# Kernel optimization log

Hardware: AMD Instinct MI355X
Metric: run time of the kernel (lower is better)

The kernel has to match this reference:

```python
import jax, jax.numpy as jnp
import numpy as np

N_HEADS = 16


def _rotate_half(x):
    x_even = x[..., ::2]
    x_odd = x[..., 1::2]
    return jnp.stack((-x_odd, x_even), axis=-1).reshape(x.shape)


def _apply_rope(x, cos, sin):
    # cos/sin: (S, d_head) broadcast against (B, H, S, d_head)
    return x * cos + _rotate_half(x) * sin


def setup_inputs() -> dict:
    key = jax.random.key(0)
    k1, k2, k3 = jax.random.split(key, 3)
    B, S, D, H = 2, 2048, 1024, N_HEADS
    dh = D // H
    x = jax.random.normal(k1, (B, S, D), dtype=jnp.float32)
    w_qkv = jax.random.normal(k2, (D, 3 * D), dtype=jnp.float32) * 0.02
    w_proj = jax.random.normal(k3, (D, D), dtype=jnp.float32) * 0.02
    # standard interleaved RoPE tables, shape (S, d_head)
    inv_freq = 1.0 / (10000.0 ** (jnp.arange(0, dh, 2, dtype=jnp.float32) / dh))
    angles = jnp.arange(S, dtype=jnp.float32)[:, None] * inv_freq[None, :]  # (S, dh/2)
    rope_cos = jnp.repeat(jnp.cos(angles), 2, axis=-1)  # (S, dh)
    rope_sin = jnp.repeat(jnp.sin(angles), 2, axis=-1)
    return {"x": x, "w_qkv": w_qkv, "w_proj": w_proj, "rope_cos": rope_cos, "rope_sin": rope_sin}


def reference(x, w_qkv, w_proj, rope_cos, rope_sin):
    B, S, D = x.shape
    H = N_HEADS
    dh = D // H
    half = dh // 2
    qkv = x @ w_qkv  # (B, S, 3D)
    q, k, v = jnp.split(qkv, 3, axis=-1)
    # (B, S, D) -> (B, H, S, dh)
    q = q.reshape(B, S, H, dh).transpose(0, 2, 1, 3)
    k = k.reshape(B, S, H, dh).transpose(0, 2, 1, 3)
    v = v.reshape(B, S, H, dh).transpose(0, 2, 1, 3)
    q = _apply_rope(q, rope_cos, rope_sin)
    k = _apply_rope(k, rope_cos, rope_sin)
    scale = half ** -0.5
    # dual score matrices from the two half-subspaces
    attn_up = jnp.einsum('bhid,bhjd->bhij', q[..., :half], k[..., :half]) * scale
    attn_down = jnp.einsum('bhid,bhjd->bhij', q[..., half:], k[..., half:]) * scale
    lower_mask = jnp.tril(jnp.ones((S, S), dtype=bool))  # j <= i -> down
    attn_logits = jnp.where(lower_mask, attn_down, attn_up)
    attn_weights = jax.nn.softmax(attn_logits, axis=-1)
    attn_out = jnp.einsum('bhij,bhjd->bhid', attn_weights, v)
    attn_out = attn_out.transpose(0, 2, 1, 3).reshape(B, S, D)
    return attn_out @ w_proj
```

## Files before the change

kernel.cpp:

```cpp
#include <hip/hip_runtime.h>
#include <hip/hip_bf16.h>
#include <stdint.h>

typedef __bf16 bf16;
typedef __attribute__((ext_vector_type(4))) __bf16 bf16x4;
typedef __attribute__((ext_vector_type(8))) __bf16 bf16x8;
typedef __attribute__((ext_vector_type(4))) float f32x4;

#define MFMA16(a, b, c) __builtin_amdgcn_mfma_f32_16x16x32_bf16((a), (b), (c), 0, 0, 0)

#define QSC (0.17677669529663687f * 1.4426950408889634f)

__device__ __forceinline__ void async_cp16(const bf16* g, bf16* l) {
  __builtin_amdgcn_global_load_lds(
      (const __attribute__((address_space(1))) void*)g,
      (__attribute__((address_space(3))) void*)l, 16, 0, 0);
}

__global__ __launch_bounds__(256) void convx_k(const float* __restrict__ in,
                                               bf16* __restrict__ out, int n) {
  int i = (blockIdx.x * 256 + threadIdx.x) * 4;
  const int stride = gridDim.x * 256 * 4;
  for (; i < n; i += stride) {
    const f32x4 f = *(const f32x4*)(in + i);
    bf16x4 o;
    o[0] = (bf16)f[0]; o[1] = (bf16)f[1]; o[2] = (bf16)f[2]; o[3] = (bf16)f[3];
    *(bf16x4*)(out + i) = o;
  }
}

__global__ __launch_bounds__(256) void transpose_k(const float* __restrict__ in,
                                                   bf16* __restrict__ out, int R, int C) {
  __shared__ bf16 t[64][65];
  const int bc = blockIdx.x * 64;
  const int br = blockIdx.y * 64;
  const int tx = threadIdx.x & 63, ty = threadIdx.x >> 6;
#pragma unroll
  for (int r = ty; r < 64; r += 4) t[r][tx] = (bf16)in[(br + r) * C + bc + tx];
  __syncthreads();
#pragma unroll
  for (int r = ty; r < 64; r += 4) out[(bc + r) * R + br + tx] = t[tx][r];
}

template <int MODE, int BM>
__global__ __launch_bounds__(256) void gemm128(
    const bf16* __restrict__ A, const bf16* __restrict__ BT, int M, int N, int K,
    float* __restrict__ C, bf16* __restrict__ qws, bf16* __restrict__ kws,
    bf16* __restrict__ vT, const float* __restrict__ ropeC, const float* __restrict__ ropeS) {
  constexpr int MT = BM / 32;
  __shared__ __align__(16) bf16 As[BM * 64];
  __shared__ __align__(16) bf16 Bs[128 * 64];
  const int tid = threadIdx.x;
  const int lane = tid & 63, wave = tid >> 6;
  const int l16 = lane & 15, quad = lane >> 4;
  const int wm = (wave >> 1) * (BM / 2), wn = (wave & 1) * 64;
  const int bm = blockIdx.y, bn = blockIdx.x;

  const int srow = tid >> 3;
  const int schunk = ((tid & 7) - srow) & 7;
  const bf16* ag = A + (bm * BM + srow) * K + schunk * 8;
  const bf16* bg = BT + (bn * 128 + srow) * K + schunk * 8;
  bf16* la = &As[tid * 8];
  bf16* lb = &Bs[tid * 8];

  f32x4 acc[MT][4] = {};

  for (int k0 = 0; k0 < K; k0 += 64) {
    async_cp16(ag + k0, la);
    async_cp16(ag + 32 * K + k0, la + 2048);
    if (BM == 128) {
      async_cp16(ag + 64 * K + k0, la + 4096);
      async_cp16(ag + 96 * K + k0, la + 6144);
    }
    async_cp16(bg + k0, lb);
    async_cp16(bg + 32 * K + k0, lb + 2048);
    async_cp16(bg + 64 * K + k0, lb + 4096);
    async_cp16(bg + 96 * K + k0, lb + 6144);
    __syncthreads();
#pragma unroll
    for (int ks = 0; ks < 2; ++ks) {
      bf16x8 af[MT], bff[4];
#pragma unroll
      for (int t = 0; t < MT; ++t) {
        const int r = wm + t * 16 + l16;
        af[t] = *(const bf16x8*)&As[r * 64 + ((ks * 4 + quad + r) & 7) * 8];
      }
#pragma unroll
      for (int t = 0; t < 4; ++t) {
        const int r = wn + t * 16 + l16;
        bff[t] = *(const bf16x8*)&Bs[r * 64 + ((ks * 4 + quad + r) & 7) * 8];
      }
#pragma unroll
      for (int mt = 0; mt < MT; ++mt)
#pragma unroll
        for (int nt = 0; nt < 4; ++nt) acc[mt][nt] = MFMA16(af[mt], bff[nt], acc[mt][nt]);
    }
    __syncthreads();
  }

  if (MODE == 0) {
#pragma unroll
    for (int mt = 0; mt < MT; ++mt)
#pragma unroll
      for (int i = 0; i < 4; ++i) {
        const int row = bm * BM + wm + mt * 16 + quad * 4 + i;
#pragma unroll
        for (int nt = 0; nt < 4; ++nt) {
          const int col = bn * 128 + wn + nt * 16 + l16;
          C[row * N + col] = acc[mt][nt][i];
        }
      }
  } else {
    bf16* tb = &Bs[wave * 512];
#pragma unroll
    for (int mt = 0; mt < MT; ++mt) {
      const int s0 = bm * BM + wm + mt * 16;
      const int b = s0 >> 11, sbase = s0 & 2047;
#pragma unroll
      for (int nt = 0; nt < 4; ++nt) {
        const int colb = bn * 128 + wn + nt * 16;
        const int sec = colb >> 10, rem = colb & 1023;
        const int h = rem >> 6, d0 = rem & 63;
        if (sec < 2) {
          const int d = d0 + l16;
#pragma unroll
          for (int i = 0; i < 4; ++i) {
            const int s = sbase + quad * 4 + i;
            float v = acc[mt][nt][i];
            float pr = __shfl_xor(v, 1);
            float rot = (d & 1) ? pr : -pr;
            float rv = v * ropeC[s * 64 + d] + rot * ropeS[s * 64 + d];
            if (sec == 0) rv *= QSC;
            tb[(quad * 4 + i) * 20 + l16] = (bf16)rv;
          }
          bf16* dst = ((sec == 0) ? qws : kws) + ((b * 16 + h) * 2048 + sbase) * 64 + d0;
          bf16x4 seg = *(const bf16x4*)&tb[l16 * 20 + quad * 4];
          *(bf16x4*)(dst + l16 * 64 + quad * 4) = seg;
        } else {
          const int d = d0 + l16;
          const int s4 = sbase + quad * 4;
          const int a = (s4 >> 4) & 3;
          const int p = (s4 & ~63) | ((a >> 1) * 32 + quad * 8 + (a & 1) * 4);
          bf16x4 pk;
#pragma unroll
          for (int i = 0; i < 4; ++i) pk[i] = (bf16)acc[mt][nt][i];
          *(bf16x4*)(vT + ((b * 16 + h) * 64 + d) * 2048 + p) = pk;
        }
      }
    }
  }
}

__global__ __launch_bounds__(256) void attn_k(const bf16* __restrict__ qws,
                                              const bf16* __restrict__ kws,
                                              const bf16* __restrict__ vT,
                                              bf16* __restrict__ aw) {
  __shared__ __align__(16) bf16 Ks[2][64 * 64];
  __shared__ __align__(16) bf16 Vs[2][64 * 64];
  const int tid = threadIdx.x;
  const int lane = tid & 63, wave = tid >> 6;
  const int l16 = lane & 15, quad = lane >> 4;
  const int bh = blockIdx.x >> 4, qblk = blockIdx.x & 15;
  const int b = bh >> 4, h = bh & 15;
  const int rbase = qblk * 128 + wave * 32;

  const bf16* qb = qws + (bh * 2048 + rbase) * 64;
  const bf16* kb = kws + bh * 2048 * 64;
  const bf16* vb = vT + bh * 64 * 2048;

  const int r0 = wave * 16 + (lane >> 3);
  const int c0 = ((lane & 7) - r0) & 7;
  const bf16* kst0 = kb + r0 * 64 + c0 * 8;
  const bf16* kst1 = kb + (r0 + 8) * 64 + c0 * 8;
  const bf16* vst0 = vb + r0 * 2048 + c0 * 8;
  const bf16* vst1 = vb + (r0 + 8) * 2048 + c0 * 8;

#define STAGE(jtv)                                         \
  {                                                        \
    bf16* kdst = &Ks[(jtv) & 1][wave * 1024];              \
    bf16* vdst = &Vs[(jtv) & 1][wave * 1024];              \
    async_cp16(kst0 + (jtv) * 4096, kdst);                 \
    async_cp16(kst1 + (jtv) * 4096, kdst + 512);           \
    async_cp16(vst0 + (jtv) * 64, vdst);                   \
    async_cp16(vst1 + (jtv) * 64, vdst + 512);             \
  }

  bf16x8 qf[2][2];
#pragma unroll
  for (int g = 0; g < 2; ++g)
#pragma unroll
    for (int hf = 0; hf < 2; ++hf)
      qf[g][hf] = *(const bf16x8*)(qb + (g * 16 + l16) * 64 + hf * 32 + quad * 8);

  bf16x8 ones;
#pragma unroll
  for (int j = 0; j < 8; ++j) ones[j] = (bf16)1.0f;

  f32x4 o[2][4] = {};
  f32x4 o_l[2] = {};
  const f32x4 zz = {};
  const int tdw = rbase >> 6;

#define ATTN_BODY(TM, jt)                                                             \
  {                                                                                   \
    const bf16* Kb = Ks[(jt) & 1];                                                    \
    const bf16* Vb = Vs[(jt) & 1];                                                    \
    bf16x8 vf[2][4];                                                                  \
    _Pragma("unroll") for (int ks = 0; ks < 2; ++ks)                                  \
      _Pragma("unroll") for (int ntd = 0; ntd < 4; ++ntd)                             \
        vf[ks][ntd] = *(const bf16x8*)(Vb + (ntd * 16 + l16) * 64 +                   \
                                       ((ks * 4 + quad + l16) & 7) * 8);              \
    bf16x8 kfU[2][2], kfD[2][2];                                                      \
    _Pragma("unroll") for (int ks = 0; ks < 2; ++ks)                                  \
      _Pragma("unroll") for (int s = 0; s < 2; ++s) {                                 \
        const int ro = ((ks * 2 + s) * 16 + l16) * 64;                                \
        if (TM != 0) kfU[ks][s] = *(const bf16x8*)(Kb + ro + ((quad + l16) & 7) * 8); \
        if (TM != 2)                                                                  \
          kfD[ks][s] = *(const bf16x8*)(Kb + ro + ((4 + quad + l16) & 7) * 8);        \
      }                                                                               \
    if ((jt) + 1 < 32) STAGE((jt) + 1)                                                \
    _Pragma("unroll") for (int ks = 0; ks < 2; ++ks) {                                \
      f32x4 sU[2][2], sD[2][2];                                                       \
      _Pragma("unroll") for (int s = 0; s < 2; ++s)                                   \
        _Pragma("unroll") for (int g = 0; g < 2; ++g) {                               \
          if (TM != 0) sU[s][g] = MFMA16(kfU[ks][s], qf[g][0], zz);                   \
          if (TM != 2) sD[s][g] = MFMA16(kfD[ks][s], qf[g][1], zz);                   \
        }                                                                             \
      _Pragma("unroll") for (int g = 0; g < 2; ++g) {                                 \
        bf16x8 af;                                                                    \
        _Pragma("unroll") for (int s = 0; s < 2; ++s)                                 \
          _Pragma("unroll") for (int r = 0; r < 4; ++r) {                             \
            float x;                                                                  \
            if (TM == 0) x = sD[s][g][r];                                             \
            else if (TM == 2) x = sU[s][g][r];                                        \
            else {                                                                    \
              const int jcol = (jt) * 64 + (ks * 2 + s) * 16 + quad * 4 + r;          \
              x = (jcol <= rbase + g * 16 + l16) ? sD[s][g][r] : sU[s][g][r];         \
            }                                                                         \
            af[s * 4 + r] = (bf16)__builtin_amdgcn_exp2f(x);                          \
          }                                                                           \
        o_l[g] = MFMA16(af, ones, o_l[g]);                                            \
        _Pragma("unroll") for (int ntd = 0; ntd < 4; ++ntd)                           \
            o[g][ntd] = MFMA16(af, vf[ks][ntd], o[g][ntd]);                           \
      }                                                                               \
    }                                                                                 \
  }

  STAGE(0)
  for (int jt = 0; jt < 32; ++jt) {
    asm volatile("s_waitcnt vmcnt(0)" ::: "memory");
    __syncthreads();
    if (jt < tdw) ATTN_BODY(0, jt)
    else if (jt == tdw) ATTN_BODY(1, jt)
    else ATTN_BODY(2, jt)
  }
#undef ATTN_BODY
#undef STAGE

#pragma unroll
  for (int g = 0; g < 2; ++g) {
    float ir[4];
#pragma unroll
    for (int r = 0; r < 4; ++r) ir[r] = __builtin_amdgcn_rcpf(o_l[g][r]);
#pragma unroll
    for (int ntd = 0; ntd < 4; ++ntd)
#pragma unroll
      for (int r = 0; r < 4; ++r)
        aw[(b * 2048 + rbase + g * 16 + quad * 4 + r) * 1024 + h * 64 + ntd * 16 + l16] =
            (bf16)(o[g][ntd][r] * ir[r]);
  }
}

extern "C" void kernel_launch(void* const* d_in, const int* in_sizes, int n_in,
                              void* d_out, int out_size, void* d_ws, size_t ws_size,
                              hipStream_t stream) {
  const float* x = (const float*)d_in[0];
  const float* w_qkv = (const float*)d_in[1];
  const float* w_proj = (const float*)d_in[2];
  const float* ropeC = (const float*)d_in[3];
  const float* ropeS = (const float*)d_in[4];
  float* out = (float*)d_out;

  char* ws = (char*)d_ws;
  bf16* xb = (bf16*)ws;     ws += (size_t)4194304 * 2;
  bf16* wqkvT = (bf16*)ws;  ws += (size_t)3145728 * 2;
  bf16* wprojT = (bf16*)ws; ws += (size_t)1048576 * 2;
  bf16* qws = (bf16*)ws;    ws += (size_t)4194304 * 2;
  bf16* kws = (bf16*)ws;    ws += (size_t)4194304 * 2;
  bf16* vT = (bf16*)ws;     ws += (size_t)4194304 * 2;
  bf16* aw = (bf16*)ws;     ws += (size_t)4194304 * 2;

  convx_k<<<1024, 256, 0, stream>>>(x, xb, 4194304);
  transpose_k<<<dim3(3072 / 64, 1024 / 64), 256, 0, stream>>>(w_qkv, wqkvT, 1024, 3072);
  transpose_k<<<dim3(1024 / 64, 1024 / 64), 256, 0, stream>>>(w_proj, wprojT, 1024, 1024);

  gemm128<1, 128><<<dim3(3072 / 128, 4096 / 128), 256, 0, stream>>>(
      xb, wqkvT, 4096, 3072, 1024, nullptr, qws, kws, vT, ropeC, ropeS);
  attn_k<<<512, 256, 0, stream>>>(qws, kws, vT, aw);
  gemm128<0, 64><<<dim3(1024 / 128, 4096 / 64), 256, 0, stream>>>(
      aw, wprojT, 4096, 1024, 1024, out, nullptr, nullptr, nullptr, nullptr, nullptr);
}
```

Before: 196.0 us.

## Fuse prep kernels into one launch and halve attention rows per block

```diff
diff --git a/kernel.cpp b/kernel.cpp
--- a/kernel.cpp
+++ b/kernel.cpp
@@ -17,23 +17,32 @@
       (__attribute__((address_space(3))) void*)l, 16, 0, 0);
 }
 
-__global__ __launch_bounds__(256) void convx_k(const float* __restrict__ in,
-                                               bf16* __restrict__ out, int n) {
-  int i = (blockIdx.x * 256 + threadIdx.x) * 4;
-  const int stride = gridDim.x * 256 * 4;
-  for (; i < n; i += stride) {
-    const f32x4 f = *(const f32x4*)(in + i);
-    bf16x4 o;
-    o[0] = (bf16)f[0]; o[1] = (bf16)f[1]; o[2] = (bf16)f[2]; o[3] = (bf16)f[3];
-    *(bf16x4*)(out + i) = o;
-  }
-}
-
-__global__ __launch_bounds__(256) void transpose_k(const float* __restrict__ in,
-                                                   bf16* __restrict__ out, int R, int C) {
+__global__ __launch_bounds__(256) void prep_k(const float* __restrict__ x,
+                                              bf16* __restrict__ xb,
+                                              const float* __restrict__ wqkv,
+                                              bf16* __restrict__ wqkvT,
+                                              const float* __restrict__ wproj,
+                                              bf16* __restrict__ wprojT) {
   __shared__ bf16 t[64][65];
-  const int bc = blockIdx.x * 64;
-  const int br = blockIdx.y * 64;
+  const int bid = blockIdx.x;
+  if (bid < 1024) {
+    int i = (bid * 256 + threadIdx.x) * 4;
+    const int stride = 1024 * 256 * 4;
+    for (; i < 4194304; i += stride) {
+      const f32x4 f = *(const f32x4*)(x + i);
+      bf16x4 o;
+      o[0] = (bf16)f[0]; o[1] = (bf16)f[1]; o[2] = (bf16)f[2]; o[3] = (bf16)f[3];
+      *(bf16x4*)(xb + i) = o;
+    }
+    return;
+  }
+  const float* in;
+  bf16* out;
+  int R, C, tb;
+  if (bid < 1792) { in = wqkv; out = wqkvT; R = 1024; C = 3072; tb = bid - 1024; }
+  else            { in = wproj; out = wprojT; R = 1024; C = 1024; tb = bid - 1792; }
+  const int tilesx = C >> 6;
+  const int bc = (tb % tilesx) * 64, br = (tb / tilesx) * 64;
   const int tx = threadIdx.x & 63, ty = threadIdx.x >> 6;
 #pragma unroll
   for (int r = ty; r < 64; r += 4) t[r][tx] = (bf16)in[(br + r) * C + bc + tx];
@@ -160,9 +169,9 @@
   const int tid = threadIdx.x;
   const int lane = tid & 63, wave = tid >> 6;
   const int l16 = lane & 15, quad = lane >> 4;
-  const int bh = blockIdx.x >> 4, qblk = blockIdx.x & 15;
+  const int bh = blockIdx.x >> 5, qblk = blockIdx.x & 31;
   const int b = bh >> 4, h = bh & 15;
-  const int rbase = qblk * 128 + wave * 32;
+  const int rbase = qblk * 64 + wave * 16;
 
   const bf16* qb = qws + (bh * 2048 + rbase) * 64;
   const bf16* kb = kws + bh * 2048 * 64;
@@ -185,21 +194,19 @@
     async_cp16(vst1 + (jtv) * 64, vdst + 512);             \
   }
 
-  bf16x8 qf[2][2];
-#pragma unroll
-  for (int g = 0; g < 2; ++g)
-#pragma unroll
-    for (int hf = 0; hf < 2; ++hf)
-      qf[g][hf] = *(const bf16x8*)(qb + (g * 16 + l16) * 64 + hf * 32 + quad * 8);
+  bf16x8 qf[2];
+#pragma unroll
+  for (int hf = 0; hf < 2; ++hf)
+    qf[hf] = *(const bf16x8*)(qb + l16 * 64 + hf * 32 + quad * 8);
 
   bf16x8 ones;
 #pragma unroll
   for (int j = 0; j < 8; ++j) ones[j] = (bf16)1.0f;
 
-  f32x4 o[2][4] = {};
-  f32x4 o_l[2] = {};
+  f32x4 o[4] = {};
+  f32x4 o_l = {};
   const f32x4 zz = {};
-  const int tdw = rbase >> 6;
+  const int tdw = qblk;
 
 #define ATTN_BODY(TM, jt)                                                             \
   {                                                                                   \
@@ -220,29 +227,26 @@
       }                                                                               \
     if ((jt) + 1 < 32) STAGE((jt) + 1)                                                \
     _Pragma("unroll") for (int ks = 0; ks < 2; ++ks) {                                \
-      f32x4 sU[2][2], sD[2][2];                                                       \
+      f32x4 sU[2], sD[2];                                                             \
+      _Pragma("unroll") for (int s = 0; s < 2; ++s) {                                 \
+        if (TM != 0) sU[s] = MFMA16(kfU[ks][s], qf[0], zz);                           \
+        if (TM != 2) sD[s] = MFMA16(kfD[ks][s], qf[1], zz);                           \
+      }                                                                               \
+      bf16x8 af;                                                                      \
       _Pragma("unroll") for (int s = 0; s < 2; ++s)                                   \
-        _Pragma("unroll") for (int g = 0; g < 2; ++g) {                               \
-          if (TM != 0) sU[s][g] = MFMA16(kfU[ks][s], qf[g][0], zz);                   \
-          if (TM != 2) sD[s][g] = MFMA16(kfD[ks][s], qf[g][1], zz);                   \
+        _Pragma("unroll") for (int r = 0; r < 4; ++r) {                               \
+          float x;                                                                    \
+          if (TM == 0) x = sD[s][r];                                                  \
+          else if (TM == 2) x = sU[s][r];                                             \
+          else {                                                                      \
+            const int jcol = (jt) * 64 + (ks * 2 + s) * 16 + quad * 4 + r;            \
+            x = (jcol <= rbase + l16) ? sD[s][r] : sU[s][r];                          \
+          }                                                                           \
+          af[s * 4 + r] = (bf16)__builtin_amdgcn_exp2f(x);                            \
         }                                                                             \
-      _Pragma("unroll") for (int g = 0; g < 2; ++g) {                                 \
-        bf16x8 af;                                                                    \
-        _Pragma("unroll") for (int s = 0; s < 2; ++s)                                 \
-          _Pragma("unroll") for (int r = 0; r < 4; ++r) {                             \
-            float x;                                                                  \
-            if (TM == 0) x = sD[s][g][r];                                             \
-            else if (TM == 2) x = sU[s][g][r];                                        \
-            else {                                                                    \
-              const int jcol = (jt) * 64 + (ks * 2 + s) * 16 + quad * 4 + r;          \
-              x = (jcol <= rbase + g * 16 + l16) ? sD[s][g][r] : sU[s][g][r];         \
-            }                                                                         \
-            af[s * 4 + r] = (bf16)__builtin_amdgcn_exp2f(x);                          \
-          }                                                                           \
-        o_l[g] = MFMA16(af, ones, o_l[g]);                                            \
-        _Pragma("unroll") for (int ntd = 0; ntd < 4; ++ntd)                           \
-            o[g][ntd] = MFMA16(af, vf[ks][ntd], o[g][ntd]);                           \
-      }                                                                               \
+      o_l = MFMA16(af, ones, o_l);                                                    \
+      _Pragma("unroll") for (int ntd = 0; ntd < 4; ++ntd)                             \
+          o[ntd] = MFMA16(af, vf[ks][ntd], o[ntd]);                                   \
     }                                                                                 \
   }
 
@@ -257,18 +261,15 @@
 #undef ATTN_BODY
 #undef STAGE
 
-#pragma unroll
-  for (int g = 0; g < 2; ++g) {
-    float ir[4];
-#pragma unroll
-    for (int r = 0; r < 4; ++r) ir[r] = __builtin_amdgcn_rcpf(o_l[g][r]);
-#pragma unroll
-    for (int ntd = 0; ntd < 4; ++ntd)
-#pragma unroll
-      for (int r = 0; r < 4; ++r)
-        aw[(b * 2048 + rbase + g * 16 + quad * 4 + r) * 1024 + h * 64 + ntd * 16 + l16] =
-            (bf16)(o[g][ntd][r] * ir[r]);
-  }
+  float ir[4];
+#pragma unroll
+  for (int r = 0; r < 4; ++r) ir[r] = __builtin_amdgcn_rcpf(o_l[r]);
+#pragma unroll
+  for (int ntd = 0; ntd < 4; ++ntd)
+#pragma unroll
+    for (int r = 0; r < 4; ++r)
+      aw[(b * 2048 + rbase + quad * 4 + r) * 1024 + h * 64 + ntd * 16 + l16] =
+          (bf16)(o[ntd][r] * ir[r]);
 }
 
 extern "C" void kernel_launch(void* const* d_in, const int* in_sizes, int n_in,
@@ -290,13 +291,10 @@
   bf16* vT = (bf16*)ws;     ws += (size_t)4194304 * 2;
   bf16* aw = (bf16*)ws;     ws += (size_t)4194304 * 2;
 
-  convx_k<<<1024, 256, 0, stream>>>(x, xb, 4194304);
-  transpose_k<<<dim3(3072 / 64, 1024 / 64), 256, 0, stream>>>(w_qkv, wqkvT, 1024, 3072);
-  transpose_k<<<dim3(1024 / 64, 1024 / 64), 256, 0, stream>>>(w_proj, wprojT, 1024, 1024);
-
+  prep_k<<<2048, 256, 0, stream>>>(x, xb, w_qkv, wqkvT, w_proj, wprojT);
   gemm128<1, 128><<<dim3(3072 / 128, 4096 / 128), 256, 0, stream>>>(
       xb, wqkvT, 4096, 3072, 1024, nullptr, qws, kws, vT, ropeC, ropeS);
-  attn_k<<<512, 256, 0, stream>>>(qws, kws, vT, aw);
+  attn_k<<<1024, 256, 0, stream>>>(qws, kws, vT, aw);
   gemm128<0, 64><<<dim3(1024 / 128, 4096 / 64), 256, 0, stream>>>(
       aw, wprojT, 4096, 1024, 1024, out, nullptr, nullptr, nullptr, nullptr, nullptr);
 }
```

Result: no change. 195.2 us (-0.4%).
